# Kernel tuning notes

Hardware: AMD Instinct MI355X
Metric: run time of the kernel (lower is better)

Reference implementation:

```python
import jax, jax.numpy as jnp
import numpy as np

EPS = 1e-5

def _conv1x1(x, W, b):
    # x: [B,Ci,H,W], W: [Co,Ci]
    return jnp.einsum('oi,bihw->bohw', W, x) + b[None, :, None, None]

def _bn(x, gamma, beta, mean, var):
    # inference-mode BatchNorm2d
    s = gamma / jnp.sqrt(var + EPS)
    return x * s[None, :, None, None] + (beta - mean * s)[None, :, None, None]

def _conv3x3(x, W, b):
    y = jax.lax.conv_general_dilated(x, W, (1, 1), 'SAME',
                                     dimension_numbers=('NCHW', 'OIHW', 'NCHW'))
    return y + b[None, :, None, None]

def _sparsemax_last(S):
    # sparsemax over the last axis (TrackHSPA: max-subtract, sort, cumsum, threshold)
    S = S - jnp.max(S, axis=-1, keepdims=True)
    srt = -jnp.sort(-S, axis=-1)                 # descending sort
    csum = jnp.cumsum(srt, axis=-1) - 1.0
    N = S.shape[-1]
    ar = jnp.arange(1, N + 1, dtype=S.dtype)
    mask = ar * srt > csum
    k = jnp.sum(mask, axis=-1, keepdims=True)    # support size per row
    tau = jnp.take_along_axis(csum, k - 1, axis=-1) / k.astype(S.dtype)
    return jnp.maximum(S - tau, 0.0)

def _forward(zf, xf, Wq, bq, Ws, bs, Wg, bg, g_gamma, g_beta, g_mean, g_var,
             Wfi, bfi, fi_gamma, fi_beta, fi_mean, fi_var,
             Wm, bm, m_gamma, m_beta, m_mean, m_var, prelu_a):
    B, C, Hx, Wx = xf.shape
    # ---- Graph_Attention_Union (cross-attention) ----
    xf_t = _conv1x1(xf, Wq, bq).reshape(B, C, -1)      # [B,C,Nx]
    zf_t = _conv1x1(zf, Ws, bs).reshape(B, C, -1)      # [B,C,Nz]
    xf_g = jax.nn.relu(_bn(_conv1x1(xf, Wg, bg), g_gamma, g_beta, g_mean, g_var))
    zf_g = jax.nn.relu(_bn(_conv1x1(zf, Wg, bg), g_gamma, g_beta, g_mean, g_var))
    sim = jnp.einsum('bcn,bcm->bnm', xf_t, zf_t)       # [B,Nx,Nz]
    attn = jax.nn.softmax(sim, axis=2)
    emb = jnp.einsum('bcm,bnm->bcn', zf_g.reshape(B, C, -1), attn)
    emb = emb.reshape(B, C, Hx, Wx)
    gat = jax.nn.relu(_bn(_conv1x1(jnp.concatenate([emb, xf_g], axis=1), Wfi, bfi),
                          fi_gamma, fi_beta, fi_mean, fi_var))
    # ---- TrackHSPA (adaptive sparsemax self-attention) ----
    e = _conv3x3(gat, Wm, bm)
    e = _bn(e, m_gamma, m_beta, m_mean, m_var)
    e = jnp.where(e >= 0, e, prelu_a * e)              # PReLU (single param)
    N = Hx * Wx
    ef = e.reshape(B, -1, N)                           # [B,C',N]
    S = jnp.einsum('bdi,bdj->bij', ef, ef)             # [B,N,N]
    P = _sparsemax_last(S)
    out = jnp.einsum('bcn,bnm->bcm', gat.reshape(B, C, N), P)
    return out.reshape(B, C, Hx, Wx) + gat


def setup_inputs():
    key = jax.random.key(0)
    ks = jax.random.split(key, 8)
    B, C, Hz, Wz, Hx, Wx = 32, 256, 7, 7, 31, 31
    Cm = C // 4
    f = lambda k, shape: jax.random.normal(k, shape, jnp.float32) * 0.05
    return {
        'zf': jax.random.normal(ks[0], (B, C, Hz, Wz), jnp.float32),
        'xf': jax.random.normal(ks[1], (B, C, Hx, Wx), jnp.float32),
        'Wq': f(ks[2], (C, C)), 'bq': jnp.zeros((C,), jnp.float32),
        'Ws': f(ks[3], (C, C)), 'bs': jnp.zeros((C,), jnp.float32),
        'Wg': f(ks[4], (C, C)), 'bg': jnp.zeros((C,), jnp.float32),
        'g_gamma': jnp.ones((C,), jnp.float32), 'g_beta': jnp.zeros((C,), jnp.float32),
        'g_mean': jnp.zeros((C,), jnp.float32), 'g_var': jnp.ones((C,), jnp.float32),
        'Wfi': f(ks[5], (C, 2 * C)), 'bfi': jnp.zeros((C,), jnp.float32),
        'fi_gamma': jnp.ones((C,), jnp.float32), 'fi_beta': jnp.zeros((C,), jnp.float32),
        'fi_mean': jnp.zeros((C,), jnp.float32), 'fi_var': jnp.ones((C,), jnp.float32),
        'Wm': f(ks[6], (Cm, C, 3, 3)), 'bm': jnp.zeros((Cm,), jnp.float32),
        'm_gamma': jnp.ones((Cm,), jnp.float32), 'm_beta': jnp.zeros((Cm,), jnp.float32),
        'm_mean': jnp.zeros((Cm,), jnp.float32), 'm_var': jnp.ones((Cm,), jnp.float32),
        'prelu_a': jnp.array(0.25, jnp.float32),
    }


def reference(zf, xf, Wq, bq, Ws, bs, Wg, bg, g_gamma, g_beta, g_mean, g_var,
              Wfi, bfi, fi_gamma, fi_beta, fi_mean, fi_var,
              Wm, bm, m_gamma, m_beta, m_mean, m_var, prelu_a):
    return _forward(zf, xf, Wq, bq, Ws, bs, Wg, bg, g_gamma, g_beta, g_mean, g_var,
                    Wfi, bfi, fi_gamma, fi_beta, fi_mean, fi_var,
                    Wm, bm, m_gamma, m_beta, m_mean, m_var, prelu_a)
```

## Files before the change

### kernel.cpp

```cpp
#include <hip/hip_runtime.h>
#include <cstdint>
#include <cstddef>
#include <math.h>

typedef __attribute__((ext_vector_type(8))) short short8;
typedef __attribute__((ext_vector_type(4))) float floatx4;
typedef unsigned short ushort_t;

__device__ __forceinline__ ushort_t f2bf(float x) {
    union { float f; unsigned u; } v; v.f = x;
    unsigned r = v.u + 0x7FFF + ((v.u >> 16) & 1);
    return (ushort_t)(r >> 16);
}
__device__ __forceinline__ float bf2f(ushort_t h) {
    union { unsigned u; float f; } v; v.u = ((unsigned)h) << 16; return v.f;
}
__device__ __forceinline__ void split2(float v, ushort_t& h, ushort_t& l) {
    h = f2bf(v);
    l = f2bf(v - bf2f(h));
}

#define MFMA(a, b, c) __builtin_amdgcn_mfma_f32_16x16x32_bf16((a), (b), (c), 0, 0, 0)

__device__ __forceinline__ void gload_lds16(const void* g, void* l) {
    __builtin_amdgcn_global_load_lds(
        (const __attribute__((address_space(1))) unsigned*)g,
        (__attribute__((address_space(3))) unsigned*)l, 16, 0, 0);
}

__global__ void prep_all_kernel(
    const float* __restrict__ Wq, const float* __restrict__ Ws,
    const float* __restrict__ Wg, const float* __restrict__ Wfi,
    const float* __restrict__ Wm,
    const float* bq, const float* bs,
    const float* bg, const float* gg, const float* gb, const float* gm, const float* gv,
    const float* bfi, const float* fg, const float* fb, const float* fm, const float* fv,
    const float* bm, const float* mg, const float* mb, const float* mm, const float* mv,
    ushort_t* Wq_h, ushort_t* Wq_l, ushort_t* Ws_h, ushort_t* Ws_l,
    ushort_t* Wg_h, ushort_t* Wg_l, ushort_t* Wfi_h, ushort_t* Wfi_l,
    ushort_t* wm_h, ushort_t* wm_l, float* scsh)
{
    int bid = blockIdx.x, t = threadIdx.x;
    if (bid < 256) {
        int i = bid * 256 + t; ushort_t h, l; split2(Wq[i], h, l); Wq_h[i] = h; Wq_l[i] = l;
    } else if (bid < 512) {
        int i = (bid - 256) * 256 + t; ushort_t h, l; split2(Ws[i], h, l); Ws_h[i] = h; Ws_l[i] = l;
    } else if (bid < 768) {
        int i = (bid - 512) * 256 + t; ushort_t h, l; split2(Wg[i], h, l); Wg_h[i] = h; Wg_l[i] = l;
    } else if (bid < 1280) {
        int i = (bid - 768) * 256 + t; ushort_t h, l; split2(Wfi[i], h, l); Wfi_h[i] = h; Wfi_l[i] = l;
    } else if (bid < 1856) {
        int i = (bid - 1280) * 256 + t;
        int c = i & 255, m = (i >> 8) & 63, tap = i >> 14;
        ushort_t h, l; split2(Wm[((size_t)m * 256 + c) * 9 + tap], h, l);
        wm_h[i] = h; wm_l[i] = l;
    } else {
        if (t < 256) {
            scsh[t] = 1.f;        scsh[256 + t] = bq[t];
            scsh[512 + t] = 1.f;  scsh[768 + t] = bs[t];
            float s = gg[t] * rsqrtf(gv[t] + 1e-5f);
            scsh[1024 + t] = s;   scsh[1280 + t] = gb[t] + s * (bg[t] - gm[t]);
            float s2 = fg[t] * rsqrtf(fv[t] + 1e-5f);
            scsh[1536 + t] = s2;  scsh[1792 + t] = fb[t] + s2 * (bfi[t] - fm[t]);
            if (t < 64) {
                float s3 = mg[t] * rsqrtf(mv[t] + 1e-5f);
                scsh[2048 + t] = s3; scsh[2112 + t] = mb[t] + s3 * (bm[t] - mm[t]);
            }
        }
    }
}

__global__ void halo_zero_kernel(ushort_t* __restrict__ gxh, ushort_t* __restrict__ gxl) {
    int i = blockIdx.x * 256 + threadIdx.x;
    int b = i >> 7, k = i & 127;
    int r;
    if (k < 33) r = k;
    else if (k < 66) r = 32 * 33 + (k - 33);
    else { int k2 = k - 66; r = ((k2 >> 1) + 1) * 33 + ((k2 & 1) ? 32 : 0); }
    uint4* ph = (uint4*)(gxh + ((size_t)b * 1089 + r) * 256);
    uint4* pl = (uint4*)(gxl + ((size_t)b * 1089 + r) * 256);
    uint4 z = make_uint4(0, 0, 0, 0);
#pragma unroll
    for (int s = 0; s < 32; s++) { ph[s] = z; pl[s] = z; }
}

__global__ __launch_bounds__(256) void transpose_in_kernel(
    const float* __restrict__ in, ushort_t* __restrict__ oh, ushort_t* __restrict__ ol,
    int Nsrc, int Npad)
{
    int b = blockIdx.z;
    const float* ib = in + (size_t)b * 256 * Nsrc;
    ushort_t* obh = oh + (size_t)b * Npad * 256;
    ushort_t* obl = ol + (size_t)b * Npad * 256;
    __shared__ float tile[32][33];
    int n0 = blockIdx.x * 32, c0 = blockIdx.y * 32;
    int tx = threadIdx.x & 31, ty = threadIdx.x >> 5;
#pragma unroll
    for (int r = 0; r < 4; r++) {
        int c = c0 + ty + r * 8, n = n0 + tx;
        tile[ty + r * 8][tx] = (n < Nsrc) ? ib[(size_t)c * Nsrc + n] : 0.f;
    }
    __syncthreads();
#pragma unroll
    for (int r = 0; r < 4; r++) {
        int n = n0 + ty + r * 8, c = c0 + tx;
        if (n < Nsrc) {
            ushort_t h, l; split2(tile[tx][ty + r * 8], h, l);
            obh[(size_t)n * 256 + c] = h;
            obl[(size_t)n * 256 + c] = l;
        }
    }
}

__global__ __launch_bounds__(256, 2) void dualconv_mfma_kernel(
    const ushort_t* __restrict__ Xh, const ushort_t* __restrict__ Xl,
    const ushort_t* __restrict__ W1h, const ushort_t* __restrict__ W1l,
    const ushort_t* __restrict__ W2h, const ushort_t* __restrict__ W2l,
    const float* __restrict__ sc1, const float* __restrict__ sh1,
    const float* __restrict__ sc2, const float* __restrict__ sh2,
    int relu1, int relu2,
    ushort_t* __restrict__ O1h, ushort_t* __restrict__ O1l,
    ushort_t* __restrict__ O2h, ushort_t* __restrict__ O2l,
    ushort_t* __restrict__ O2ch, ushort_t* __restrict__ O2cl, int cpitch,
    int K, int Nvalid, int NpadIn, int NpadOut)
{
    __shared__ ushort_t Bs[16384];
    int b = blockIdx.x;
    int n0 = blockIdx.y * 32;
    const ushort_t* Xbh = Xh + (size_t)b * NpadIn * K;
    const ushort_t* Xbl = Xl + (size_t)b * NpadIn * K;
    int tid = threadIdx.x, w = tid >> 6, l = tid & 63, lc = l & 15, q = l >> 4;
    int m0 = w * 64;

#pragma unroll
    for (int r = 0; r < 8; r++) {
        int d = r * 4096 + w * 1024 + l * 16;
        int seg = d >> 14;
        int dr = d & 16383;
        int row = dr >> 9;
        int inrow = (dr & 511) ^ ((row & 7) << 4);
        int srow = n0 + row; if (srow > NpadIn - 1) srow = NpadIn - 1;
        const ushort_t* src = (seg ? Xbl : Xbh) + (size_t)srow * K + (inrow >> 1);
        char* dst = (char*)Bs + (r * 4096 + w * 1024);
        gload_lds16(src, dst);
    }
    __syncthreads();

#define DC_LOADA(K0, AH, AL) do { \
    _Pragma("unroll") \
    for (int mt_ = 0; mt_ < 4; mt_++) { \
        size_t off_ = (size_t)(m0 + mt_ * 16 + lc) * K + (K0) + q * 8; \
        AH[mt_] = *(const short8*)(Wh + off_); \
        AL[mt_] = *(const short8*)(Wl + off_); \
    } \
} while (0)
#define DC_LDSB(K0, BH, BL) do { \
    _Pragma("unroll") \
    for (int jt_ = 0; jt_ < 2; jt_++) { \
        int row_ = jt_ * 16 + lc; \
        int koff_ = (((K0) + q * 8) * 2) ^ ((row_ & 7) << 4); \
        BH[jt_] = *(const short8*)((const char*)Bs + row_ * 512 + koff_); \
        BL[jt_] = *(const short8*)((const char*)Bs + 16384 + row_ * 512 + koff_); \
    } \
} while (0)
#define DC_MFMA(AH, AL, BH, BL) do { \
    _Pragma("unroll") \
    for (int mt_ = 0; mt_ < 4; mt_++) \
    _Pragma("unroll") \
    for (int jt_ = 0; jt_ < 2; jt_++) { \
        acc[mt_][jt_] = MFMA(AH[mt_], BH[jt_], acc[mt_][jt_]); \
        acc[mt_][jt_] = MFMA(AH[mt_], BL[jt_], acc[mt_][jt_]); \
        acc[mt_][jt_] = MFMA(AL[mt_], BH[jt_], acc[mt_][jt_]); \
    } \
} while (0)

    for (int half = 0; half < 2; half++) {
        const ushort_t* Wh = half ? W2h : W1h;
        const ushort_t* Wl = half ? W2l : W1l;
        const float* sc = half ? sc2 : sc1;
        const float* sh = half ? sh2 : sh1;
        int relu = half ? relu2 : relu1;
        ushort_t* Obh = (half ? O2h : O1h) + (size_t)b * NpadOut * 256;
        ushort_t* Obl = (half ? O2l : O1l) + (size_t)b * NpadOut * 256;

        floatx4 acc[4][2];
#pragma unroll
        for (int i = 0; i < 4; i++)
#pragma unroll
            for (int j = 0; j < 2; j++) acc[i][j] = (floatx4){0.f, 0.f, 0.f, 0.f};

        short8 ah0[4], al0[4], ah1[4], al1[4], bh[2], bl[2];
        DC_LOADA(0, ah0, al0);
        for (int k0 = 0; k0 < K; k0 += 64) {
            DC_LOADA(k0 + 32, ah1, al1);
            DC_LDSB(k0, bh, bl);
            DC_MFMA(ah0, al0, bh, bl);
            if (k0 + 64 < K) DC_LOADA(k0 + 64, ah0, al0);
            DC_LDSB(k0 + 32, bh, bl);
            DC_MFMA(ah1, al1, bh, bl);
        }

#pragma unroll
        for (int mt = 0; mt < 4; mt++) {
            int mb = m0 + mt * 16 + q * 4;
            float s0 = sc[mb], s1 = sc[mb + 1], s2 = sc[mb + 2], s3 = sc[mb + 3];
            float h0 = sh[mb], h1 = sh[mb + 1], h2 = sh[mb + 2], h3 = sh[mb + 3];
#pragma unroll
            for (int jt = 0; jt < 2; jt++) {
                int n = n0 + jt * 16 + lc;
                if (n >= Nvalid) continue;
                float v0 = acc[mt][jt][0] * s0 + h0;
                float v1 = acc[mt][jt][1] * s1 + h1;
                float v2 = acc[mt][jt][2] * s2 + h2;
                float v3 = acc[mt][jt][3] * s3 + h3;
                if (relu) { v0 = fmaxf(v0, 0.f); v1 = fmaxf(v1, 0.f); v2 = fmaxf(v2, 0.f); v3 = fmaxf(v3, 0.f); }
                ushort_t e0, f0, e1, f1, e2, f2, e3, f3;
                split2(v0, e0, f0); split2(v1, e1, f1); split2(v2, e2, f2); split2(v3, e3, f3);
                *(ushort4*)(Obh + (size_t)n * 256 + mb) = make_ushort4(e0, e1, e2, e3);
                *(ushort4*)(Obl + (size_t)n * 256 + mb) = make_ushort4(f0, f1, f2, f3);
                if (half && O2ch) {
                    O2ch[((size_t)b * 256 + mb + 0) * cpitch + n] = e0;
                    O2ch[((size_t)b * 256 + mb + 1) * cpitch + n] = e1;
                    O2ch[((size_t)b * 256 + mb + 2) * cpitch + n] = e2;
                    O2ch[((size_t)b * 256 + mb + 3) * cpitch + n] = e3;
                    O2cl[((size_t)b * 256 + mb + 0) * cpitch + n] = f0;
                    O2cl[((size_t)b * 256 + mb + 1) * cpitch + n] = f1;
                    O2cl[((size_t)b * 256 + mb + 2) * cpitch + n] = f2;
                    O2cl[((size_t)b * 256 + mb + 3) * cpitch + n] = f3;
                }
            }
        }
    }
#undef DC_LOADA
#undef DC_LDSB
#undef DC_MFMA
}

__global__ __launch_bounds__(256) void attn_mfma_kernel(
    const ushort_t* __restrict__ xth, const ushort_t* __restrict__ xtl,
    const ushort_t* __restrict__ zth, const ushort_t* __restrict__ ztl,
    const ushort_t* __restrict__ zgh, const ushort_t* __restrict__ zgl,
    ushort_t* __restrict__ eh, ushort_t* __restrict__ el)
{
    __shared__ float S[64][68];
    __shared__ ushort_t awh[64][72], awl[64][72];
    __shared__ float T[4][16][20];
    int b = blockIdx.x, n0 = blockIdx.y * 64;
    int tid = threadIdx.x, w = tid >> 6, l = tid & 63, lc = l & 15, q = l >> 4;
    const ushort_t* xhb = xth + (size_t)b * 992 * 256;
    const ushort_t* xlb = xtl + (size_t)b * 992 * 256;
    const ushort_t* zhb = zth + (size_t)b * 64 * 256;
    const ushort_t* zlb = ztl + (size_t)b * 64 * 256;
    const ushort_t* ghb = zgh + (size_t)b * 256 * 64;
    const ushort_t* glb = zgl + (size_t)b * 256 * 64;

    int rowg = n0 + w * 16 + lc;
#pragma unroll
    for (int ct = 0; ct < 4; ct++) {
        floatx4 acc = (floatx4){0.f, 0.f, 0.f, 0.f};
        for (int k0 = 0; k0 < 256; k0 += 32) {
            short8 ah = *(const short8*)(xhb + (size_t)rowg * 256 + k0 + q * 8);
            short8 al = *(const short8*)(xlb + (size_t)rowg * 256 + k0 + q * 8);
            short8 bh = *(const short8*)(zhb + (size_t)(ct * 16 + lc) * 256 + k0 + q * 8);
            short8 bl = *(const short8*)(zlb + (size_t)(ct * 16 + lc) * 256 + k0 + q * 8);
            acc = MFMA(ah, bh, acc);
            acc = MFMA(ah, bl, acc);
            acc = MFMA(al, bh, acc);
        }
#pragma unroll
        for (int r = 0; r < 4; r++) S[w * 16 + q * 4 + r][ct * 16 + lc] = acc[r];
    }
    __syncthreads();
    if (tid < 64) {
        float mx = -INFINITY;
        for (int m = 0; m < 49; m++) mx = fmaxf(mx, S[tid][m]);
        float sum = 0.f;
        for (int m = 0; m < 49; m++) { float e = __expf(S[tid][m] - mx); S[tid][m] = e; sum += e; }
        float inv = 1.f / sum;
        for (int m = 0; m < 64; m++) {
            float vv = (m < 49) ? S[tid][m] * inv : 0.f;
            ushort_t hh, ll; split2(vv, hh, ll);
            awh[tid][m] = hh; awl[tid][m] = ll;
        }
    }
    __syncthreads();
    int nw = l >> 2, cg = l & 3;
#pragma unroll
    for (int ct = 0; ct < 16; ct++) {
        floatx4 acc = (floatx4){0.f, 0.f, 0.f, 0.f};
#pragma unroll
        for (int k0 = 0; k0 < 64; k0 += 32) {
            short8 ah = *(const short8*)(&awh[w * 16 + lc][k0 + q * 8]);
            short8 al = *(const short8*)(&awl[w * 16 + lc][k0 + q * 8]);
            short8 bh = *(const short8*)(ghb + (size_t)(ct * 16 + lc) * 64 + k0 + q * 8);
            short8 bl = *(const short8*)(glb + (size_t)(ct * 16 + lc) * 64 + k0 + q * 8);
            acc = MFMA(ah, bh, acc);
            acc = MFMA(ah, bl, acc);
            acc = MFMA(al, bh, acc);
        }
#pragma unroll
        for (int r = 0; r < 4; r++) T[w][q * 4 + r][lc] = acc[r];
        float4 vv = *(const float4*)&T[w][nw][cg * 4];
        int n = n0 + w * 16 + nw;
        if (n < 961) {
            ushort_t h0, l0, h1, l1, h2, l2_, h3, l3;
            split2(vv.x, h0, l0); split2(vv.y, h1, l1);
            split2(vv.z, h2, l2_); split2(vv.w, h3, l3);
            size_t off = ((size_t)b * 992 + n) * 256 + ct * 16 + cg * 4;
            *(ushort4*)(eh + off) = make_ushort4(h0, h1, h2, h3);
            *(ushort4*)(el + off) = make_ushort4(l0, l1, l2_, l3);
        }
    }
}

__global__ __launch_bounds__(256, 2) void fi_mfma_kernel(
    const ushort_t* __restrict__ Eh, const ushort_t* __restrict__ El,
    const ushort_t* __restrict__ Gh, const ushort_t* __restrict__ Gl,
    const ushort_t* __restrict__ Wh, const ushort_t* __restrict__ Wl,
    const float* __restrict__ sc, const float* __restrict__ sh,
    ushort_t* __restrict__ gxh, ushort_t* __restrict__ gxl,
    ushort_t* __restrict__ gat_nf)
{
    __shared__ ushort_t Bs[16384];
    int b = blockIdx.x;
    const ushort_t* Ebh = Eh + (size_t)b * 992 * 256;
    const ushort_t* Ebl = El + (size_t)b * 992 * 256;
    const ushort_t* Gbh = Gh + (size_t)b * 992 * 256;
    const ushort_t* Gbl = Gl + (size_t)b * 992 * 256;
    ushort_t* gxhb = gxh + (size_t)b * 1089 * 256;
    ushort_t* gxlb = gxl + (size_t)b * 1089 * 256;
    ushort_t* gn = gat_nf + (size_t)b * 256 * 992;
    int tid = threadIdx.x, w = tid >> 6, l = tid & 63, lc = l & 15, q = l >> 4;
    int m0 = w * 64, nb0 = blockIdx.y * 32;

    floatx4 acc[4][2];
#pragma unroll
    for (int i = 0; i < 4; i++)
#pragma unroll
        for (int j = 0; j < 2; j++) acc[i][j] = (floatx4){0.f, 0.f, 0.f, 0.f};

#define FI_LOADA(K0, AH, AL) do { \
    _Pragma("unroll") \
    for (int mt_ = 0; mt_ < 4; mt_++) { \
        size_t off_ = (size_t)(m0 + mt_ * 16 + lc) * 512 + (K0) + q * 8; \
        AH[mt_] = *(const short8*)(Wh + off_); \
        AL[mt_] = *(const short8*)(Wl + off_); \
    } \
} while (0)
#define FI_LDSB(K0, BH, BL) do { \
    _Pragma("unroll") \
    for (int jt_ = 0; jt_ < 2; jt_++) { \
        int row_ = jt_ * 16 + lc; \
        int koff_ = (((K0) + q * 8) * 2) ^ ((row_ & 7) << 4); \
        BH[jt_] = *(const short8*)((const char*)Bs + row_ * 512 + koff_); \
        BL[jt_] = *(const short8*)((const char*)Bs + 16384 + row_ * 512 + koff_); \
    } \
} while (0)
#define FI_MFMA(AH, AL, BH, BL) do { \
    _Pragma("unroll") \
    for (int mt_ = 0; mt_ < 4; mt_++) \
    _Pragma("unroll") \
    for (int jt_ = 0; jt_ < 2; jt_++) { \
        acc[mt_][jt_] = MFMA(AH[mt_], BH[jt_], acc[mt_][jt_]); \
        acc[mt_][jt_] = MFMA(AH[mt_], BL[jt_], acc[mt_][jt_]); \
        acc[mt_][jt_] = MFMA(AL[mt_], BH[jt_], acc[mt_][jt_]); \
    } \
} while (0)

    for (int p = 0; p < 2; p++) {
        const ushort_t* srcH = p ? Gbh : Ebh;
        const ushort_t* srcL = p ? Gbl : Ebl;
        if (p) __syncthreads();
#pragma unroll
        for (int r = 0; r < 8; r++) {
            int d = r * 4096 + w * 1024 + l * 16;
            int seg = d >> 14;
            int dr = d & 16383;
            int row = dr >> 9;
            int inrow = (dr & 511) ^ ((row & 7) << 4);
            int srow = nb0 + row; if (srow > 991) srow = 991;
            const ushort_t* src = (seg ? srcL : srcH) + (size_t)srow * 256 + (inrow >> 1);
            char* dst = (char*)Bs + (r * 4096 + w * 1024);
            gload_lds16(src, dst);
        }
        __syncthreads();

        int pb = p * 256;
        short8 ah0[4], al0[4], ah1[4], al1[4], bh[2], bl[2];
        FI_LOADA(pb, ah0, al0);
        for (int kk = 0; kk < 256; kk += 64) {
            FI_LOADA(pb + kk + 32, ah1, al1);
            FI_LDSB(kk, bh, bl);
            FI_MFMA(ah0, al0, bh, bl);
            if (kk + 64 < 256) FI_LOADA(pb + kk + 64, ah0, al0);
            FI_LDSB(kk + 32, bh, bl);
            FI_MFMA(ah1, al1, bh, bl);
        }
    }
#undef FI_LOADA
#undef FI_LDSB
#undef FI_MFMA

#pragma unroll
    for (int mt = 0; mt < 4; mt++) {
        int mb = m0 + mt * 16 + q * 4;
        float s0 = sc[mb], s1 = sc[mb + 1], s2 = sc[mb + 2], s3 = sc[mb + 3];
        float h0 = sh[mb], h1 = sh[mb + 1], h2 = sh[mb + 2], h3 = sh[mb + 3];
#pragma unroll
        for (int jt = 0; jt < 2; jt++) {
            int n = nb0 + jt * 16 + lc;
            if (n >= 961) continue;
            float v0 = fmaxf(acc[mt][jt][0] * s0 + h0, 0.f);
            float v1 = fmaxf(acc[mt][jt][1] * s1 + h1, 0.f);
            float v2 = fmaxf(acc[mt][jt][2] * s2 + h2, 0.f);
            float v3 = fmaxf(acc[mt][jt][3] * s3 + h3, 0.f);
            ushort_t a0, b0, a1, b1, a2, b2, a3, b3;
            split2(v0, a0, b0); split2(v1, a1, b1); split2(v2, a2, b2); split2(v3, a3, b3);
            int hh = n / 31, ww2 = n - hh * 31;
            int row = (hh + 1) * 33 + (ww2 + 1);
            *(ushort4*)(gxhb + (size_t)row * 256 + mb) = make_ushort4(a0, a1, a2, a3);
            *(ushort4*)(gxlb + (size_t)row * 256 + mb) = make_ushort4(b0, b1, b2, b3);
            gn[(size_t)(mb + 0) * 992 + n] = a0;
            gn[(size_t)(mb + 1) * 992 + n] = a1;
            gn[(size_t)(mb + 2) * 992 + n] = a2;
            gn[(size_t)(mb + 3) * 992 + n] = a3;
        }
    }
}

__global__ __launch_bounds__(256, 2) void conv3x3_mfma_kernel(
    const ushort_t* __restrict__ gxh, const ushort_t* __restrict__ gxl,
    const ushort_t* __restrict__ wmh, const ushort_t* __restrict__ wml,
    const float* __restrict__ sc, const float* __restrict__ sh,
    const float* __restrict__ prelu_a,
    ushort_t* __restrict__ eh, ushort_t* __restrict__ el)
{
    __shared__ float Sp[4][2048];
    int b = blockIdx.x;
    const ushort_t* gxhb = gxh + (size_t)b * 1089 * 256;
    const ushort_t* gxlb = gxl + (size_t)b * 1089 * 256;
    ushort_t* ebh = eh + (size_t)b * 1024 * 64;
    ushort_t* ebl = el + (size_t)b * 1024 * 64;
    int tid = threadIdx.x, w = tid >> 6, l = tid & 63, lc = l & 15, q = l >> 4;
    int j0 = blockIdx.y * 64;

    int base[4];
#pragma unroll
    for (int jt = 0; jt < 4; jt++) {
        int j = j0 + jt * 16 + lc; if (j > 960) j = 960;
        int hh = j / 31, ww2 = j - hh * 31;
        base[jt] = (hh + 1) * 33 + (ww2 + 1);
    }

    floatx4 acc[4][4];
#pragma unroll
    for (int i = 0; i < 4; i++)
#pragma unroll
        for (int j = 0; j < 4; j++) acc[i][j] = (floatx4){0.f, 0.f, 0.f, 0.f};

#define C3_LOAD(SL, AH, AL, BH, BL) do { \
    int sl_ = (SL); \
    int tap_ = (sl_ >= 9) ? sl_ - 9 : sl_; \
    int k0_ = (w * 2 + ((sl_ >= 9) ? 1 : 0)) * 32; \
    int doff_ = (tap_ / 3 - 1) * 33 + (tap_ % 3 - 1); \
    const ushort_t* wth_ = wmh + tap_ * 16384; \
    const ushort_t* wtl_ = wml + tap_ * 16384; \
    _Pragma("unroll") \
    for (int mt_ = 0; mt_ < 4; mt_++) { \
        size_t off_ = (size_t)(mt_ * 16 + lc) * 256 + k0_ + q * 8; \
        AH[mt_] = *(const short8*)(wth_ + off_); \
        AL[mt_] = *(const short8*)(wtl_ + off_); \
    } \
    _Pragma("unroll") \
    for (int jt_ = 0; jt_ < 4; jt_++) { \
        size_t off_ = (size_t)(base[jt_] + doff_) * 256 + k0_ + q * 8; \
        BH[jt_] = *(const short8*)(gxhb + off_); \
        BL[jt_] = *(const short8*)(gxlb + off_); \
    } \
} while (0)
#define C3_MFMA(AH, AL, BH, BL) do { \
    _Pragma("unroll") \
    for (int mt_ = 0; mt_ < 4; mt_++) \
    _Pragma("unroll") \
    for (int jt_ = 0; jt_ < 4; jt_++) { \
        acc[mt_][jt_] = MFMA(AH[mt_], BH[jt_], acc[mt_][jt_]); \
        acc[mt_][jt_] = MFMA(AH[mt_], BL[jt_], acc[mt_][jt_]); \
        acc[mt_][jt_] = MFMA(AL[mt_], BH[jt_], acc[mt_][jt_]); \
    } \
} while (0)

    short8 A0h[4], A0l[4], B0h[4], B0l[4];
    short8 A1h[4], A1l[4], B1h[4], B1l[4];
    C3_LOAD(0, A0h, A0l, B0h, B0l);
#pragma unroll
    for (int it = 0; it < 9; it++) {
        C3_LOAD(it * 2 + 1, A1h, A1l, B1h, B1l);
        C3_MFMA(A0h, A0l, B0h, B0l);
        if (it < 8) C3_LOAD(it * 2 + 2, A0h, A0l, B0h, B0l);
        C3_MFMA(A1h, A1l, B1h, B1l);
    }
#undef C3_LOAD
#undef C3_MFMA

    float pa = prelu_a[0];
#pragma unroll
    for (int ph = 0; ph < 2; ph++) {
        __syncthreads();
#pragma unroll
        for (int mt = 0; mt < 4; mt++)
#pragma unroll
            for (int jt = 0; jt < 2; jt++)
#pragma unroll
                for (int r = 0; r < 4; r++)
                    Sp[w][(mt * 16 + q * 4 + r) * 32 + jt * 16 + lc] = acc[mt][ph * 2 + jt][r];
        __syncthreads();
#pragma unroll
        for (int gi = 0; gi < 2; gi++) {
            int g = tid + gi * 256;
            int j = g & 31, mg = g >> 5;
            int m = mg * 4;
            int jj = j0 + ph * 32 + j;
            if (jj >= 961) continue;
            float v[4];
#pragma unroll
            for (int i = 0; i < 4; i++) {
                int idx = (m + i) * 32 + j;
                v[i] = Sp[0][idx] + Sp[1][idx] + Sp[2][idx] + Sp[3][idx];
                v[i] = v[i] * sc[m + i] + sh[m + i];
                v[i] = v[i] >= 0.f ? v[i] : pa * v[i];
            }
            ushort_t a0, b0, a1, b1, a2, b2, a3, b3;
            split2(v[0], a0, b0); split2(v[1], a1, b1);
            split2(v[2], a2, b2); split2(v[3], a3, b3);
            *(ushort4*)(ebh + (size_t)jj * 64 + m) = make_ushort4(a0, a1, a2, a3);
            *(ushort4*)(ebl + (size_t)jj * 64 + m) = make_ushort4(b0, b1, b2, b3);
        }
    }
}

__global__ __launch_bounds__(512) void hspa_mfma_kernel(
    const ushort_t* __restrict__ eh, const ushort_t* __restrict__ el,
    ushort_t* __restrict__ PT)
{
    const int PITCH = 978;
    __shared__ float S[16 * 978];
    int b = blockIdx.x, nb = blockIdx.y;
    const ushort_t* ebh = eh + (size_t)b * 1024 * 64;
    const ushort_t* ebl = el + (size_t)b * 1024 * 64;
    ushort_t* Pb = PT + (size_t)b * 1024 * 992;
    int tid = threadIdx.x, w = tid >> 6, l = tid & 63, lc = l & 15, q = l >> 4;
    int n0 = nb * 32;

    short8 Ah[2][2], Al[2][2];
#pragma unroll
// ... 75 lines not shown
#pragma unroll
        for (int t = 0; t < 16; t++) { sv0[t] -= mx0; sv1[t] -= mx1; }

        float tau0 = -1.f, tau1 = -1.f;
        for (int it = 0; it < 16; it++) {
            float s0 = 0.f, c0 = 0.f, s1 = 0.f, c1 = 0.f;
#pragma unroll
            for (int t = 0; t < 16; t++) {
                if (sv0[t] > tau0) { s0 += sv0[t]; c0 += 1.f; }
                if (sv1[t] > tau1) { s1 += sv1[t]; c1 += 1.f; }
            }
            for (int off = 32; off; off >>= 1) {
                s0 += __shfl_xor(s0, off); c0 += __shfl_xor(c0, off);
                s1 += __shfl_xor(s1, off); c1 += __shfl_xor(c1, off);
            }
            float nt0 = (s0 - 1.f) / c0;
            float nt1 = (s1 - 1.f) / c1;
            bool conv = (nt0 == tau0) && (nt1 == tau1);
            tau0 = nt0; tau1 = nt1;
            if (conv) break;
        }
#pragma unroll
        for (int t = 0; t < 16; t++) {
            int j = l + t * 64;
            if (j < 976) {
                S[r0 * PITCH + j] = (j < 961) ? fmaxf(sv0[t] - tau0, 0.f) : 0.f;
                S[r1 * PITCH + j] = (j < 961) ? fmaxf(sv1[t] - tau1, 0.f) : 0.f;
            }
        }
        __syncthreads();

        int nbase = n0 + g * 16;
        if (nbase < 976) {
            for (int j = tid; j < 976; j += 512) {
                union { ushort_t u[8]; uint4 v; } p0, p1;
#pragma unroll
                for (int r = 0; r < 8; r++)  p0.u[r] = f2bf(S[r * PITCH + j]);
#pragma unroll
                for (int r = 0; r < 8; r++)  p1.u[r] = f2bf(S[(8 + r) * PITCH + j]);
                ushort_t* dst = Pb + (size_t)j * 992 + nbase;
                *(uint4*)(dst) = p0.v;
                *(uint4*)(dst + 8) = p1.v;
            }
        }
    }
}

__global__ __launch_bounds__(256, 2) void out_mfma_kernel(
    const ushort_t* __restrict__ gat_nf, const ushort_t* __restrict__ PT,
    float* __restrict__ out)
{
    int b = blockIdx.x, jb = blockIdx.y;
    const ushort_t* gb = gat_nf + (size_t)b * 256 * 992;
    const ushort_t* Pb = PT + (size_t)b * 1024 * 992;
    float* ob = out + (size_t)b * 256 * 961;
    int tid = threadIdx.x, w = tid >> 6, l = tid & 63, lc = l & 15, q = l >> 4;
    int m0 = w * 64, j0 = jb * 64;

    floatx4 acc[4][4];
#pragma unroll
    for (int i = 0; i < 4; i++)
#pragma unroll
        for (int j = 0; j < 4; j++) acc[i][j] = (floatx4){0.f, 0.f, 0.f, 0.f};

#define OUT_LOAD(K0, AA, BB) do { \
    _Pragma("unroll") \
    for (int mt_ = 0; mt_ < 4; mt_++) \
        AA[mt_] = *(const short8*)(gb + (size_t)(m0 + mt_ * 16 + lc) * 992 + (K0) + q * 8); \
    _Pragma("unroll") \
    for (int jt_ = 0; jt_ < 4; jt_++) \
        BB[jt_] = *(const short8*)(Pb + (size_t)(j0 + jt_ * 16 + lc) * 992 + (K0) + q * 8); \
} while (0)
#define OUT_MFMA(AA, BB) do { \
    _Pragma("unroll") \
    for (int mt_ = 0; mt_ < 4; mt_++) \
    _Pragma("unroll") \
    for (int jt_ = 0; jt_ < 4; jt_++) \
        acc[mt_][jt_] = MFMA(AA[mt_], BB[jt_], acc[mt_][jt_]); \
} while (0)

    short8 a0[4], b0[4], a1[4], b1[4];
    OUT_LOAD(0, a0, b0);
    for (int k0 = 0; k0 < 960; k0 += 64) {
        OUT_LOAD(k0 + 32, a1, b1);
        OUT_MFMA(a0, b0);
        OUT_LOAD(k0 + 64, a0, b0);
        OUT_MFMA(a1, b1);
    }
    OUT_MFMA(a0, b0);
#undef OUT_LOAD
#undef OUT_MFMA

#pragma unroll
    for (int mt = 0; mt < 4; mt++) {
        int mb = m0 + mt * 16 + q * 4;
#pragma unroll
        for (int jt = 0; jt < 4; jt++) {
            int j = j0 + jt * 16 + lc;
            if (j >= 961) continue;
#pragma unroll
            for (int r = 0; r < 4; r++) {
                float g = bf2f(gb[(size_t)(mb + r) * 992 + j]);
                ob[(size_t)(mb + r) * 961 + j] = acc[mt][jt][r] + g;
            }
        }
    }
}

extern "C" void kernel_launch(void* const* d_in, const int* in_sizes, int n_in,
                              void* d_out, int out_size, void* d_ws, size_t ws_size,
                              hipStream_t stream)
{
    const float* zf      = (const float*)d_in[0];
    const float* xf      = (const float*)d_in[1];
    const float* Wq      = (const float*)d_in[2];
    const float* bq      = (const float*)d_in[3];
    const float* Ws      = (const float*)d_in[4];
    const float* bs      = (const float*)d_in[5];
    const float* Wg      = (const float*)d_in[6];
    const float* bg      = (const float*)d_in[7];
    const float* g_gamma = (const float*)d_in[8];
    const float* g_beta  = (const float*)d_in[9];
    const float* g_mean  = (const float*)d_in[10];
    const float* g_var   = (const float*)d_in[11];
    const float* Wfi     = (const float*)d_in[12];
    const float* bfi     = (const float*)d_in[13];
    const float* fi_gamma= (const float*)d_in[14];
    const float* fi_beta = (const float*)d_in[15];
    const float* fi_mean = (const float*)d_in[16];
    const float* fi_var  = (const float*)d_in[17];
    const float* Wm      = (const float*)d_in[18];
    const float* bm      = (const float*)d_in[19];
    const float* m_gamma = (const float*)d_in[20];
    const float* m_beta  = (const float*)d_in[21];
    const float* m_mean  = (const float*)d_in[22];
    const float* m_var   = (const float*)d_in[23];
    const float* prelu_a = (const float*)d_in[24];
    float* out = (float*)d_out;

    ushort_t* ws = (ushort_t*)d_ws;
    ushort_t* Wq_h  = ws + 0;         ushort_t* Wq_l  = ws + 65536;
    ushort_t* Ws_h  = ws + 131072;    ushort_t* Ws_l  = ws + 196608;
    ushort_t* Wg_h  = ws + 262144;    ushort_t* Wg_l  = ws + 327680;
    ushort_t* Wfi_h = ws + 393216;    ushort_t* Wfi_l = ws + 524288;
    ushort_t* wm_h  = ws + 655360;    ushort_t* wm_l  = ws + 802816;
    ushort_t* XT_h    = ws + 950272;
    ushort_t* XT_l    = ws + 9076736;
    ushort_t* xf_tT_h = ws + 17203200;
    ushort_t* xf_tT_l = ws + 25329664;
    ushort_t* zf_tT_h = ws + 33456128;
    ushort_t* zf_tT_l = ws + 33980416;
    ushort_t* zf_gT_h = ws + 34504704;
    ushort_t* zf_gT_l = ws + 35028992;
    ushort_t* gxT_h   = ws + 17203200;
    ushort_t* gxT_l   = ws + 26124288;
    ushort_t* xf_gT_h = ws + 35553280;
    ushort_t* xf_gT_l = ws + 43679744;
    ushort_t* gat_nf  = ws + 51806208;
    ushort_t* eT_h    = ws + 59932672;
    ushort_t* eT_l    = ws + 62029824;
    ushort_t* PT      = ws + 64126976;
    ushort_t* zfT_h   = ws + 96632832;
    ushort_t* zfT_l   = ws + 97157120;
    float* scsh       = (float*)(ws + 97681408);
    ushort_t* zgC_h   = ws + 97685760;
    ushort_t* zgC_l   = ws + 98210048;
    ushort_t* embT_h = XT_h;
    ushort_t* embT_l = XT_l;

    const float* sc_q  = scsh + 0,    *sh_q  = scsh + 256;
    const float* sc_s  = scsh + 512,  *sh_s  = scsh + 768;
    const float* sc_g  = scsh + 1024, *sh_g  = scsh + 1280;
    const float* sc_fi = scsh + 1536, *sh_fi = scsh + 1792;
    const float* sc_m  = scsh + 2048, *sh_m  = scsh + 2112;

    prep_all_kernel<<<1857, 256, 0, stream>>>(
        Wq, Ws, Wg, Wfi, Wm,
        bq, bs, bg, g_gamma, g_beta, g_mean, g_var,
        bfi, fi_gamma, fi_beta, fi_mean, fi_var,
        bm, m_gamma, m_beta, m_mean, m_var,
        Wq_h, Wq_l, Ws_h, Ws_l, Wg_h, Wg_l, Wfi_h, Wfi_l, wm_h, wm_l, scsh);

    transpose_in_kernel<<<dim3(31, 8, 32), 256, 0, stream>>>(xf, XT_h, XT_l, 961, 992);
    transpose_in_kernel<<<dim3(2, 8, 32), 256, 0, stream>>>(zf, zfT_h, zfT_l, 49, 64);

    dualconv_mfma_kernel<<<dim3(32, 31), 256, 0, stream>>>(
        XT_h, XT_l, Wq_h, Wq_l, Wg_h, Wg_l,
        sc_q, sh_q, sc_g, sh_g, 0, 1,
        xf_tT_h, xf_tT_l, xf_gT_h, xf_gT_l,
        nullptr, nullptr, 0, 256, 961, 992, 992);
    dualconv_mfma_kernel<<<dim3(32, 2), 256, 0, stream>>>(
        zfT_h, zfT_l, Ws_h, Ws_l, Wg_h, Wg_l,
        sc_s, sh_s, sc_g, sh_g, 0, 1,
        zf_tT_h, zf_tT_l, zf_gT_h, zf_gT_l,
        zgC_h, zgC_l, 64, 256, 49, 64, 64);

    attn_mfma_kernel<<<dim3(32, 16), 256, 0, stream>>>(
        xf_tT_h, xf_tT_l, zf_tT_h, zf_tT_l, zgC_h, zgC_l, embT_h, embT_l);

    halo_zero_kernel<<<16, 256, 0, stream>>>(gxT_h, gxT_l);

    fi_mfma_kernel<<<dim3(32, 31), 256, 0, stream>>>(
        embT_h, embT_l, xf_gT_h, xf_gT_l, Wfi_h, Wfi_l, sc_fi, sh_fi,
        gxT_h, gxT_l, gat_nf);

    conv3x3_mfma_kernel<<<dim3(32, 16), 256, 0, stream>>>(
        gxT_h, gxT_l, wm_h, wm_l, sc_m, sh_m, prelu_a, eT_h, eT_l);

    hspa_mfma_kernel<<<dim3(32, 31), 512, 0, stream>>>(eT_h, eT_l, PT);

    out_mfma_kernel<<<dim3(32, 16), 256, 0, stream>>>(gat_nf, PT, out);
}
```

Measured before the change: 567.6 us.

## Fuse attention into fi conv kernel and split dualconv halves across blocks

The cross-attention softmax and embedding computation now live inside the fi 1x1-conv kernel. The embedding tile goes straight into LDS as the B operand, so the separate attention kernel and its global round trip for emb are gone. The dualconv kernel now gives each output half to its own block (grid y doubled, launch bounds raised to 4 waves per SIMD) instead of looping over both halves, for more parallelism. The cost is that the input tile is loaded twice in dualconv and the workspace aliasing changes, with gxT moved to overlap PT.

```diff
diff --git a/kernel.cpp b/kernel.cpp
--- a/kernel.cpp
+++ b/kernel.cpp
@@ -112,7 +112,7 @@
     }
 }
 
-__global__ __launch_bounds__(256, 2) void dualconv_mfma_kernel(
+__global__ __launch_bounds__(256, 4) void dualconv_mfma_kernel(
     const ushort_t* __restrict__ Xh, const ushort_t* __restrict__ Xl,
     const ushort_t* __restrict__ W1h, const ushort_t* __restrict__ W1l,
     const ushort_t* __restrict__ W2h, const ushort_t* __restrict__ W2l,
@@ -126,7 +126,8 @@
 {
     __shared__ ushort_t Bs[16384];
     int b = blockIdx.x;
-    int n0 = blockIdx.y * 32;
+    int half = blockIdx.y & 1;
+    int n0 = (blockIdx.y >> 1) * 32;
     const ushort_t* Xbh = Xh + (size_t)b * NpadIn * K;
     const ushort_t* Xbl = Xl + (size_t)b * NpadIn * K;
     int tid = threadIdx.x, w = tid >> 6, l = tid & 63, lc = l & 15, q = l >> 4;
@@ -146,6 +147,14 @@
     }
     __syncthreads();
 
+    const ushort_t* Wh = half ? W2h : W1h;
+    const ushort_t* Wl = half ? W2l : W1l;
+    const float* sc = half ? sc2 : sc1;
+    const float* sh = half ? sh2 : sh1;
+    int relu = half ? relu2 : relu1;
+    ushort_t* Obh = (half ? O2h : O1h) + (size_t)b * NpadOut * 256;
+    ushort_t* Obl = (half ? O2l : O1l) + (size_t)b * NpadOut * 256;
+
 #define DC_LOADA(K0, AH, AL) do { \
     _Pragma("unroll") \
     for (int mt_ = 0; mt_ < 4; mt_++) { \
@@ -174,21 +183,13 @@
     } \
 } while (0)
 
-    for (int half = 0; half < 2; half++) {
-        const ushort_t* Wh = half ? W2h : W1h;
-        const ushort_t* Wl = half ? W2l : W1l;
-        const float* sc = half ? sc2 : sc1;
-        const float* sh = half ? sh2 : sh1;
-        int relu = half ? relu2 : relu1;
-        ushort_t* Obh = (half ? O2h : O1h) + (size_t)b * NpadOut * 256;
-        ushort_t* Obl = (half ? O2l : O1l) + (size_t)b * NpadOut * 256;
-
-        floatx4 acc[4][2];
-#pragma unroll
-        for (int i = 0; i < 4; i++)
-#pragma unroll
-            for (int j = 0; j < 2; j++) acc[i][j] = (floatx4){0.f, 0.f, 0.f, 0.f};
-
+    floatx4 acc[4][2];
+#pragma unroll
+    for (int i = 0; i < 4; i++)
+#pragma unroll
+        for (int j = 0; j < 2; j++) acc[i][j] = (floatx4){0.f, 0.f, 0.f, 0.f};
+
+    {
         short8 ah0[4], al0[4], ah1[4], al1[4], bh[2], bl[2];
         DC_LOADA(0, ah0, al0);
         for (int k0 = 0; k0 < K; k0 += 64) {
@@ -199,53 +200,58 @@
             DC_LDSB(k0 + 32, bh, bl);
             DC_MFMA(ah1, al1, bh, bl);
         }
-
-#pragma unroll
-        for (int mt = 0; mt < 4; mt++) {
-            int mb = m0 + mt * 16 + q * 4;
-            float s0 = sc[mb], s1 = sc[mb + 1], s2 = sc[mb + 2], s3 = sc[mb + 3];
-            float h0 = sh[mb], h1 = sh[mb + 1], h2 = sh[mb + 2], h3 = sh[mb + 3];
-#pragma unroll
-            for (int jt = 0; jt < 2; jt++) {
-                int n = n0 + jt * 16 + lc;
-                if (n >= Nvalid) continue;
-                float v0 = acc[mt][jt][0] * s0 + h0;
-                float v1 = acc[mt][jt][1] * s1 + h1;
-                float v2 = acc[mt][jt][2] * s2 + h2;
-                float v3 = acc[mt][jt][3] * s3 + h3;
-                if (relu) { v0 = fmaxf(v0, 0.f); v1 = fmaxf(v1, 0.f); v2 = fmaxf(v2, 0.f); v3 = fmaxf(v3, 0.f); }
-                ushort_t e0, f0, e1, f1, e2, f2, e3, f3;
-                split2(v0, e0, f0); split2(v1, e1, f1); split2(v2, e2, f2); split2(v3, e3, f3);
-                *(ushort4*)(Obh + (size_t)n * 256 + mb) = make_ushort4(e0, e1, e2, e3);
-                *(ushort4*)(Obl + (size_t)n * 256 + mb) = make_ushort4(f0, f1, f2, f3);
-                if (half && O2ch) {
-                    O2ch[((size_t)b * 256 + mb + 0) * cpitch + n] = e0;
-                    O2ch[((size_t)b * 256 + mb + 1) * cpitch + n] = e1;
-                    O2ch[((size_t)b * 256 + mb + 2) * cpitch + n] = e2;
-                    O2ch[((size_t)b * 256 + mb + 3) * cpitch + n] = e3;
-                    O2cl[((size_t)b * 256 + mb + 0) * cpitch + n] = f0;
-                    O2cl[((size_t)b * 256 + mb + 1) * cpitch + n] = f1;
-                    O2cl[((size_t)b * 256 + mb + 2) * cpitch + n] = f2;
-                    O2cl[((size_t)b * 256 + mb + 3) * cpitch + n] = f3;
-                }
-            }
-        }
     }
 #undef DC_LOADA
 #undef DC_LDSB
 #undef DC_MFMA
-}
-
-__global__ __launch_bounds__(256) void attn_mfma_kernel(
+
+#pragma unroll
+    for (int mt = 0; mt < 4; mt++) {
+        int mb = m0 + mt * 16 + q * 4;
+        float s0 = sc[mb], s1 = sc[mb + 1], s2 = sc[mb + 2], s3 = sc[mb + 3];
+        float h0 = sh[mb], h1 = sh[mb + 1], h2 = sh[mb + 2], h3 = sh[mb + 3];
+#pragma unroll
+        for (int jt = 0; jt < 2; jt++) {
+            int n = n0 + jt * 16 + lc;
+            if (n >= Nvalid) continue;
+            float v0 = acc[mt][jt][0] * s0 + h0;
+            float v1 = acc[mt][jt][1] * s1 + h1;
+            float v2 = acc[mt][jt][2] * s2 + h2;
+            float v3 = acc[mt][jt][3] * s3 + h3;
+            if (relu) { v0 = fmaxf(v0, 0.f); v1 = fmaxf(v1, 0.f); v2 = fmaxf(v2, 0.f); v3 = fmaxf(v3, 0.f); }
+            ushort_t e0, f0, e1, f1, e2, f2, e3, f3;
+            split2(v0, e0, f0); split2(v1, e1, f1); split2(v2, e2, f2); split2(v3, e3, f3);
+            *(ushort4*)(Obh + (size_t)n * 256 + mb) = make_ushort4(e0, e1, e2, e3);
+            *(ushort4*)(Obl + (size_t)n * 256 + mb) = make_ushort4(f0, f1, f2, f3);
+            if (half && O2ch) {
+                O2ch[((size_t)b * 256 + mb + 0) * cpitch + n] = e0;
+                O2ch[((size_t)b * 256 + mb + 1) * cpitch + n] = e1;
+                O2ch[((size_t)b * 256 + mb + 2) * cpitch + n] = e2;
+                O2ch[((size_t)b * 256 + mb + 3) * cpitch + n] = e3;
+                O2cl[((size_t)b * 256 + mb + 0) * cpitch + n] = f0;
+                O2cl[((size_t)b * 256 + mb + 1) * cpitch + n] = f1;
+                O2cl[((size_t)b * 256 + mb + 2) * cpitch + n] = f2;
+                O2cl[((size_t)b * 256 + mb + 3) * cpitch + n] = f3;
+            }
+        }
+    }
+}
+
+__global__ __launch_bounds__(256, 2) void attnfi_mfma_kernel(
     const ushort_t* __restrict__ xth, const ushort_t* __restrict__ xtl,
     const ushort_t* __restrict__ zth, const ushort_t* __restrict__ ztl,
     const ushort_t* __restrict__ zgh, const ushort_t* __restrict__ zgl,
-    ushort_t* __restrict__ eh, ushort_t* __restrict__ el)
+    const ushort_t* __restrict__ Gh, const ushort_t* __restrict__ Gl,
+    const ushort_t* __restrict__ Wh, const ushort_t* __restrict__ Wl,
+    const float* __restrict__ sc, const float* __restrict__ sh,
+    ushort_t* __restrict__ gxh, ushort_t* __restrict__ gxl,
+    ushort_t* __restrict__ gat_nf)
 {
-    __shared__ float S[64][68];
-    __shared__ ushort_t awh[64][72], awl[64][72];
-    __shared__ float T[4][16][20];
-    int b = blockIdx.x, n0 = blockIdx.y * 64;
+    __shared__ float SM[32][68];
+    __shared__ ushort_t AWh[32][72], AWl[32][72];
+    __shared__ ushort_t EM[16384];
+
+    int b = blockIdx.x, nb0 = blockIdx.y * 32;
     int tid = threadIdx.x, w = tid >> 6, l = tid & 63, lc = l & 15, q = l >> 4;
     const ushort_t* xhb = xth + (size_t)b * 992 * 256;
     const ushort_t* xlb = xtl + (size_t)b * 992 * 256;
@@ -253,93 +259,83 @@
     const ushort_t* zlb = ztl + (size_t)b * 64 * 256;
     const ushort_t* ghb = zgh + (size_t)b * 256 * 64;
     const ushort_t* glb = zgl + (size_t)b * 256 * 64;
-
-    int rowg = n0 + w * 16 + lc;
-#pragma unroll
-    for (int ct = 0; ct < 4; ct++) {
-        floatx4 acc = (floatx4){0.f, 0.f, 0.f, 0.f};
-        for (int k0 = 0; k0 < 256; k0 += 32) {
-            short8 ah = *(const short8*)(xhb + (size_t)rowg * 256 + k0 + q * 8);
-            short8 al = *(const short8*)(xlb + (size_t)rowg * 256 + k0 + q * 8);
-            short8 bh = *(const short8*)(zhb + (size_t)(ct * 16 + lc) * 256 + k0 + q * 8);
-            short8 bl = *(const short8*)(zlb + (size_t)(ct * 16 + lc) * 256 + k0 + q * 8);
-            acc = MFMA(ah, bh, acc);
-            acc = MFMA(ah, bl, acc);
-            acc = MFMA(al, bh, acc);
-        }
-#pragma unroll
-        for (int r = 0; r < 4; r++) S[w * 16 + q * 4 + r][ct * 16 + lc] = acc[r];
-    }
-    __syncthreads();
-    if (tid < 64) {
-        float mx = -INFINITY;
-        for (int m = 0; m < 49; m++) mx = fmaxf(mx, S[tid][m]);
-        float sum = 0.f;
-        for (int m = 0; m < 49; m++) { float e = __expf(S[tid][m] - mx); S[tid][m] = e; sum += e; }
-        float inv = 1.f / sum;
-        for (int m = 0; m < 64; m++) {
-            float vv = (m < 49) ? S[tid][m] * inv : 0.f;
-            ushort_t hh, ll; split2(vv, hh, ll);
-            awh[tid][m] = hh; awl[tid][m] = ll;
-        }
-    }
-    __syncthreads();
-    int nw = l >> 2, cg = l & 3;
-#pragma unroll
-    for (int ct = 0; ct < 16; ct++) {
-        floatx4 acc = (floatx4){0.f, 0.f, 0.f, 0.f};
-#pragma unroll
-        for (int k0 = 0; k0 < 64; k0 += 32) {
-            short8 ah = *(const short8*)(&awh[w * 16 + lc][k0 + q * 8]);
-            short8 al = *(const short8*)(&awl[w * 16 + lc][k0 + q * 8]);
-            short8 bh = *(const short8*)(ghb + (size_t)(ct * 16 + lc) * 64 + k0 + q * 8);
-            short8 bl = *(const short8*)(glb + (size_t)(ct * 16 + lc) * 64 + k0 + q * 8);
-            acc = MFMA(ah, bh, acc);
-            acc = MFMA(ah, bl, acc);
-            acc = MFMA(al, bh, acc);
-        }
-#pragma unroll
-        for (int r = 0; r < 4; r++) T[w][q * 4 + r][lc] = acc[r];
-        float4 vv = *(const float4*)&T[w][nw][cg * 4];
-        int n = n0 + w * 16 + nw;
-        if (n < 961) {
-            ushort_t h0, l0, h1, l1, h2, l2_, h3, l3;
-            split2(vv.x, h0, l0); split2(vv.y, h1, l1);
-            split2(vv.z, h2, l2_); split2(vv.w, h3, l3);
-            size_t off = ((size_t)b * 992 + n) * 256 + ct * 16 + cg * 4;
-            *(ushort4*)(eh + off) = make_ushort4(h0, h1, h2, h3);
-            *(ushort4*)(el + off) = make_ushort4(l0, l1, l2_, l3);
-        }
-    }
-}
-
-__global__ __launch_bounds__(256, 2) void fi_mfma_kernel(
-    const ushort_t* __restrict__ Eh, const ushort_t* __restrict__ El,
-    const ushort_t* __restrict__ Gh, const ushort_t* __restrict__ Gl,
-    const ushort_t* __restrict__ Wh, const ushort_t* __restrict__ Wl,
-    const float* __restrict__ sc, const float* __restrict__ sh,
-    ushort_t* __restrict__ gxh, ushort_t* __restrict__ gxl,
-    ushort_t* __restrict__ gat_nf)
-{
-    __shared__ ushort_t Bs[16384];
-    int b = blockIdx.x;
-    const ushort_t* Ebh = Eh + (size_t)b * 992 * 256;
-    const ushort_t* Ebl = El + (size_t)b * 992 * 256;
     const ushort_t* Gbh = Gh + (size_t)b * 992 * 256;
     const ushort_t* Gbl = Gl + (size_t)b * 992 * 256;
     ushort_t* gxhb = gxh + (size_t)b * 1089 * 256;
     ushort_t* gxlb = gxl + (size_t)b * 1089 * 256;
     ushort_t* gn = gat_nf + (size_t)b * 256 * 992;
-    int tid = threadIdx.x, w = tid >> 6, l = tid & 63, lc = l & 15, q = l >> 4;
-    int m0 = w * 64, nb0 = blockIdx.y * 32;
-
-    floatx4 acc[4][2];
-#pragma unroll
-    for (int i = 0; i < 4; i++)
-#pragma unroll
-        for (int j = 0; j < 2; j++) acc[i][j] = (floatx4){0.f, 0.f, 0.f, 0.f};
-
-#define FI_LOADA(K0, AH, AL) do { \
+    int m0 = w * 64;
+
+    {
+        int rg = w >> 1, c2 = (w & 1) * 2;
+        size_t arow = (size_t)(nb0 + rg * 16 + lc) * 256;
+        size_t brow0 = (size_t)(c2 * 16 + lc) * 256;
+        size_t brow1 = (size_t)((c2 + 1) * 16 + lc) * 256;
+        floatx4 s0 = (floatx4){0.f, 0.f, 0.f, 0.f};
+        floatx4 s1 = (floatx4){0.f, 0.f, 0.f, 0.f};
+        for (int k0 = 0; k0 < 256; k0 += 32) {
+            short8 ah = *(const short8*)(xhb + arow + k0 + q * 8);
+            short8 al = *(const short8*)(xlb + arow + k0 + q * 8);
+            short8 b0h = *(const short8*)(zhb + brow0 + k0 + q * 8);
+            short8 b0l = *(const short8*)(zlb + brow0 + k0 + q * 8);
+            short8 b1h = *(const short8*)(zhb + brow1 + k0 + q * 8);
+            short8 b1l = *(const short8*)(zlb + brow1 + k0 + q * 8);
+            s0 = MFMA(ah, b0h, s0); s0 = MFMA(ah, b0l, s0); s0 = MFMA(al, b0h, s0);
+            s1 = MFMA(ah, b1h, s1); s1 = MFMA(ah, b1l, s1); s1 = MFMA(al, b1h, s1);
+        }
+#pragma unroll
+        for (int r = 0; r < 4; r++) {
+            SM[rg * 16 + q * 4 + r][c2 * 16 + lc] = s0[r];
+            SM[rg * 16 + q * 4 + r][(c2 + 1) * 16 + lc] = s1[r];
+        }
+    }
+    __syncthreads();
+
+    if (tid < 32) {
+        float mx = -INFINITY;
+        for (int m = 0; m < 49; m++) mx = fmaxf(mx, SM[tid][m]);
+        float sum = 0.f;
+        for (int m = 0; m < 49; m++) { float e = __expf(SM[tid][m] - mx); SM[tid][m] = e; sum += e; }
+        float inv = 1.f / sum;
+        for (int m = 0; m < 64; m++) {
+            float vv = (m < 49) ? SM[tid][m] * inv : 0.f;
+            ushort_t hh, ll; split2(vv, hh, ll);
+            AWh[tid][m] = hh; AWl[tid][m] = ll;
+        }
+    }
+    __syncthreads();
+
+#pragma unroll
+    for (int rg = 0; rg < 2; rg++) {
+        short8 pah0 = *(const short8*)(&AWh[rg * 16 + lc][q * 8]);
+        short8 pal0 = *(const short8*)(&AWl[rg * 16 + lc][q * 8]);
+        short8 pah1 = *(const short8*)(&AWh[rg * 16 + lc][32 + q * 8]);
+        short8 pal1 = *(const short8*)(&AWl[rg * 16 + lc][32 + q * 8]);
+#pragma unroll
+        for (int t = 0; t < 4; t++) {
+            int ct = w * 4 + t;
+            size_t brow = (size_t)(ct * 16 + lc) * 64;
+            short8 bh0 = *(const short8*)(ghb + brow + q * 8);
+            short8 bl0 = *(const short8*)(glb + brow + q * 8);
+            short8 bh1 = *(const short8*)(ghb + brow + 32 + q * 8);
+            short8 bl1 = *(const short8*)(glb + brow + 32 + q * 8);
+            floatx4 a = (floatx4){0.f, 0.f, 0.f, 0.f};
+            a = MFMA(pah0, bh0, a); a = MFMA(pah0, bl0, a); a = MFMA(pal0, bh0, a);
+            a = MFMA(pah1, bh1, a); a = MFMA(pah1, bl1, a); a = MFMA(pal1, bh1, a);
+            int cc = ct * 16 + lc;
+#pragma unroll
+            for (int r = 0; r < 4; r++) {
+                int n = rg * 16 + q * 4 + r;
+                int off = n * 512 + ((cc * 2) ^ ((n & 7) << 4));
+                ushort_t hh, ll; split2(a[r], hh, ll);
+                *(ushort_t*)((char*)EM + off) = hh;
+                *(ushort_t*)((char*)EM + 16384 + off) = ll;
+            }
+        }
+    }
+    __syncthreads();
+
+#define AF_LOADA(K0, AH, AL) do { \
     _Pragma("unroll") \
     for (int mt_ = 0; mt_ < 4; mt_++) { \
         size_t off_ = (size_t)(m0 + mt_ * 16 + lc) * 512 + (K0) + q * 8; \
@@ -347,16 +343,16 @@
         AL[mt_] = *(const short8*)(Wl + off_); \
     } \
 } while (0)
-#define FI_LDSB(K0, BH, BL) do { \
+#define AF_LDSB(K0, BH, BL) do { \
     _Pragma("unroll") \
     for (int jt_ = 0; jt_ < 2; jt_++) { \
         int row_ = jt_ * 16 + lc; \
         int koff_ = (((K0) + q * 8) * 2) ^ ((row_ & 7) << 4); \
-        BH[jt_] = *(const short8*)((const char*)Bs + row_ * 512 + koff_); \
-        BL[jt_] = *(const short8*)((const char*)Bs + 16384 + row_ * 512 + koff_); \
+        BH[jt_] = *(const short8*)((const char*)EM + row_ * 512 + koff_); \
+        BL[jt_] = *(const short8*)((const char*)EM + 16384 + row_ * 512 + koff_); \
     } \
 } while (0)
-#define FI_MFMA(AH, AL, BH, BL) do { \
+#define AF_MFMA(AH, AL, BH, BL) do { \
     _Pragma("unroll") \
     for (int mt_ = 0; mt_ < 4; mt_++) \
     _Pragma("unroll") \
@@ -367,39 +363,54 @@
     } \
 } while (0)
 
-    for (int p = 0; p < 2; p++) {
-        const ushort_t* srcH = p ? Gbh : Ebh;
-        const ushort_t* srcL = p ? Gbl : Ebl;
-        if (p) __syncthreads();
-#pragma unroll
-        for (int r = 0; r < 8; r++) {
-            int d = r * 4096 + w * 1024 + l * 16;
-            int seg = d >> 14;
-            int dr = d & 16383;
-            int row = dr >> 9;
-            int inrow = (dr & 511) ^ ((row & 7) << 4);
-            int srow = nb0 + row; if (srow > 991) srow = 991;
-            const ushort_t* src = (seg ? srcL : srcH) + (size_t)srow * 256 + (inrow >> 1);
-            char* dst = (char*)Bs + (r * 4096 + w * 1024);
-            gload_lds16(src, dst);
-        }
-        __syncthreads();
-
-        int pb = p * 256;
+    floatx4 acc[4][2];
+#pragma unroll
+    for (int i = 0; i < 4; i++)
+#pragma unroll
+        for (int j = 0; j < 2; j++) acc[i][j] = (floatx4){0.f, 0.f, 0.f, 0.f};
+
+    {
         short8 ah0[4], al0[4], ah1[4], al1[4], bh[2], bl[2];
-        FI_LOADA(pb, ah0, al0);
+        AF_LOADA(0, ah0, al0);
         for (int kk = 0; kk < 256; kk += 64) {
-            FI_LOADA(pb + kk + 32, ah1, al1);
-            FI_LDSB(kk, bh, bl);
-            FI_MFMA(ah0, al0, bh, bl);
-            if (kk + 64 < 256) FI_LOADA(pb + kk + 64, ah0, al0);
-            FI_LDSB(kk + 32, bh, bl);
-            FI_MFMA(ah1, al1, bh, bl);
-        }
-    }
-#undef FI_LOADA
-#undef FI_LDSB
-#undef FI_MFMA
+            AF_LOADA(kk + 32, ah1, al1);
+            AF_LDSB(kk, bh, bl);
+            AF_MFMA(ah0, al0, bh, bl);
+            if (kk + 64 < 256) AF_LOADA(kk + 64, ah0, al0);
+            AF_LDSB(kk + 32, bh, bl);
+            AF_MFMA(ah1, al1, bh, bl);
+        }
+    }
+    __syncthreads();
+
+#pragma unroll
+    for (int r = 0; r < 8; r++) {
+        int d = r * 4096 + w * 1024 + l * 16;
+        int seg = d >> 14;
+        int dr = d & 16383;
+        int row = dr >> 9;
+        int inrow = (dr & 511) ^ ((row & 7) << 4);
+        int srow = nb0 + row; if (srow > 991) srow = 991;
+        const ushort_t* src = (seg ? Gbl : Gbh) + (size_t)srow * 256 + (inrow >> 1);
+        gload_lds16(src, (char*)EM + d);
+    }
+    __syncthreads();
+
+    {
+        short8 ah0[4], al0[4], ah1[4], al1[4], bh[2], bl[2];
+        AF_LOADA(256, ah0, al0);
+        for (int kk = 0; kk < 256; kk += 64) {
+            AF_LOADA(256 + kk + 32, ah1, al1);
+            AF_LDSB(kk, bh, bl);
+            AF_MFMA(ah0, al0, bh, bl);
+            if (kk + 64 < 256) AF_LOADA(256 + kk + 64, ah0, al0);
+            AF_LDSB(kk + 32, bh, bl);
+            AF_MFMA(ah1, al1, bh, bl);
+        }
+    }
+#undef AF_LOADA
+#undef AF_LDSB
+#undef AF_MFMA
 
 #pragma unroll
     for (int mt = 0; mt < 4; mt++) {
@@ -781,21 +792,19 @@
     ushort_t* zf_tT_l = ws + 33980416;
     ushort_t* zf_gT_h = ws + 34504704;
     ushort_t* zf_gT_l = ws + 35028992;
-    ushort_t* gxT_h   = ws + 17203200;
-    ushort_t* gxT_l   = ws + 26124288;
     ushort_t* xf_gT_h = ws + 35553280;
     ushort_t* xf_gT_l = ws + 43679744;
     ushort_t* gat_nf  = ws + 51806208;
     ushort_t* eT_h    = ws + 59932672;
     ushort_t* eT_l    = ws + 62029824;
     ushort_t* PT      = ws + 64126976;
+    ushort_t* gxT_h   = ws + 64126976;
+    ushort_t* gxT_l   = ws + 73048064;
     ushort_t* zfT_h   = ws + 96632832;
     ushort_t* zfT_l   = ws + 97157120;
     float* scsh       = (float*)(ws + 97681408);
     ushort_t* zgC_h   = ws + 97685760;
     ushort_t* zgC_l   = ws + 98210048;
-    ushort_t* embT_h = XT_h;
-    ushort_t* embT_l = XT_l;
 
     const float* sc_q  = scsh + 0,    *sh_q  = scsh + 256;
     const float* sc_s  = scsh + 512,  *sh_s  = scsh + 768;
@@ -813,24 +822,22 @@
     transpose_in_kernel<<<dim3(31, 8, 32), 256, 0, stream>>>(xf, XT_h, XT_l, 961, 992);
     transpose_in_kernel<<<dim3(2, 8, 32), 256, 0, stream>>>(zf, zfT_h, zfT_l, 49, 64);
 
-    dualconv_mfma_kernel<<<dim3(32, 31), 256, 0, stream>>>(
+    dualconv_mfma_kernel<<<dim3(32, 62), 256, 0, stream>>>(
         XT_h, XT_l, Wq_h, Wq_l, Wg_h, Wg_l,
         sc_q, sh_q, sc_g, sh_g, 0, 1,
         xf_tT_h, xf_tT_l, xf_gT_h, xf_gT_l,
         nullptr, nullptr, 0, 256, 961, 992, 992);
-    dualconv_mfma_kernel<<<dim3(32, 2), 256, 0, stream>>>(
+    dualconv_mfma_kernel<<<dim3(32, 4), 256, 0, stream>>>(
         zfT_h, zfT_l, Ws_h, Ws_l, Wg_h, Wg_l,
         sc_s, sh_s, sc_g, sh_g, 0, 1,
         zf_tT_h, zf_tT_l, zf_gT_h, zf_gT_l,
         zgC_h, zgC_l, 64, 256, 49, 64, 64);
 
-    attn_mfma_kernel<<<dim3(32, 16), 256, 0, stream>>>(
-        xf_tT_h, xf_tT_l, zf_tT_h, zf_tT_l, zgC_h, zgC_l, embT_h, embT_l);
-
     halo_zero_kernel<<<16, 256, 0, stream>>>(gxT_h, gxT_l);
 
-    fi_mfma_kernel<<<dim3(32, 31), 256, 0, stream>>>(
-        embT_h, embT_l, xf_gT_h, xf_gT_l, Wfi_h, Wfi_l, sc_fi, sh_fi,
+    attnfi_mfma_kernel<<<dim3(32, 31), 256, 0, stream>>>(
+        xf_tT_h, xf_tT_l, zf_tT_h, zf_tT_l, zgC_h, zgC_l,
+        xf_gT_h, xf_gT_l, Wfi_h, Wfi_l, sc_fi, sh_fi,
         gxT_h, gxT_l, gat_nf);
 
     conv3x3_mfma_kernel<<<dim3(32, 16), 256, 0, stream>>>(
```

Measured after the change: 555.6 us. 2.1% less time.
